# Kernel tuning notes

Hardware: AMD Instinct MI355X
Metric: run time of the kernel (lower is better)

The kernel has to match this reference:

```python
import jax, jax.numpy as jnp
import numpy as np

N = 50000   # nodes
E = 640000  # edges
IN, H, OUT = 128, 128, 64
BN_EPS = 1e-5


def setup_inputs() -> dict:
    key = jax.random.key(0)
    ks = jax.random.split(key, 16)
    inp = {}
    inp["x"] = jax.random.normal(ks[0], (N, IN), jnp.float32)
    inp["edge_index"] = jax.random.randint(ks[1], (2, E), 0, N, dtype=jnp.int32)
    # BatchNorm affine params (nontrivial so grads are informative)
    inp["bn_in_gamma"] = 1.0 + 0.1 * jax.random.normal(ks[2], (IN,), jnp.float32)
    inp["bn_in_beta"] = 0.1 * jax.random.normal(ks[3], (IN,), jnp.float32)
    inp["bn1_gamma"] = 1.0 + 0.1 * jax.random.normal(ks[4], (H,), jnp.float32)
    inp["bn1_beta"] = 0.1 * jax.random.normal(ks[5], (H,), jnp.float32)
    inp["bn2_gamma"] = 1.0 + 0.1 * jax.random.normal(ks[6], (OUT,), jnp.float32)
    inp["bn2_beta"] = 0.1 * jax.random.normal(ks[7], (OUT,), jnp.float32)
    # Linear / GCNConv weights (fan-in scaled)
    inp["proj_W"] = jax.random.normal(ks[8], (IN, H), jnp.float32) / np.sqrt(IN)
    inp["proj_b"] = jnp.zeros((H,), jnp.float32)
    inp["conv1_W"] = jax.random.normal(ks[9], (H, H), jnp.float32) / np.sqrt(H)
    inp["conv1_b"] = jnp.zeros((H,), jnp.float32)
    inp["conv2_W"] = jax.random.normal(ks[10], (H, OUT), jnp.float32) / np.sqrt(H)
    inp["conv2_b"] = jnp.zeros((OUT,), jnp.float32)
    return inp


def batchnorm(x, gamma, beta):
    # training-mode BN: batch statistics (biased variance), per-feature affine
    m = jnp.mean(x, axis=0)
    v = jnp.mean(jnp.square(x - m), axis=0)
    return (x - m) * jax.lax.rsqrt(v + BN_EPS) * gamma + beta


def gcn_conv(x, src, dst, W, b):
    # PyG GCNConv: y = D^{-1/2} (A + I) D^{-1/2} (x W) + b
    xw = x @ W                                    # [N, F_out]
    loops = jnp.arange(N, dtype=src.dtype)
    s = jnp.concatenate([src, loops])             # [E + N]
    d = jnp.concatenate([dst, loops])
    deg = jax.ops.segment_sum(jnp.ones_like(d, jnp.float32), d, num_segments=N)
    dinv = jnp.where(deg > 0, jax.lax.rsqrt(deg), 0.0)
    norm = dinv[s] * dinv[d]                      # [E + N]
    msgs = xw[s] * norm[:, None]                  # gather + per-edge scale
    out = jax.ops.segment_sum(msgs, d, num_segments=N)  # scatter-add
    return out + b


def reference(x, edge_index, bn_in_gamma, bn_in_beta, bn1_gamma, bn1_beta,
              bn2_gamma, bn2_beta, proj_W, proj_b, conv1_W, conv1_b,
              conv2_W, conv2_b):
    src, dst = edge_index[0], edge_index[1]
    h = batchnorm(x, bn_in_gamma, bn_in_beta)
    h = jax.nn.relu(h @ proj_W + proj_b)
    h = jax.nn.relu(batchnorm(gcn_conv(h, src, dst, conv1_W, conv1_b),
                              bn1_gamma, bn1_beta))
    # dropout: identity in eval mode
    out = batchnorm(gcn_conv(h, src, dst, conv2_W, conv2_b),
                    bn2_gamma, bn2_beta)
    return out
```

## Files before the change

### kernel.cpp

```cpp
#include <hip/hip_runtime.h>

#define NN 50000
#define NE 640000
#define BNEPS 1e-5f
#define NBANK 16
#define CAP 64

#define OFF_CURSOR 51200
#define OFF_ESRC 102400
#define OFF_WT0 1702400
#define OFF_WT1 1710592
#define OFF_WT2 1718784
#define OFF_STATS 1726976
#define OFF_B0 1737216
#define OFF_B1 8137216

typedef __attribute__((ext_vector_type(8))) __bf16 bf16x8;
typedef __attribute__((ext_vector_type(4))) float f32x4;

__device__ __forceinline__ float uplo(unsigned int u) {
  unsigned int v = u << 16;
  return __builtin_bit_cast(float, v);
}
__device__ __forceinline__ float uphi(unsigned int u) {
  unsigned int v = u & 0xffff0000u;
  return __builtin_bit_cast(float, v);
}
__device__ __forceinline__ unsigned int f2bf(float f) {
  unsigned int u = __builtin_bit_cast(unsigned int, f);
  return (u + 0x7fffu + ((u >> 16) & 1u)) >> 16;
}

__global__ __launch_bounds__(256) void prep_k(
    const float* __restrict__ W0, const float* __restrict__ W1,
    const float* __restrict__ W2, unsigned short* __restrict__ T0,
    unsigned short* __restrict__ T1, unsigned short* __restrict__ T2,
    int* __restrict__ cursor, float* __restrict__ stats) {
  const int bid = blockIdx.x;
  const int tid = threadIdx.x;
  if (bid < 160) {
    int f = bid * 256 + tid;
    if (f < 16384) {
      int k = f >> 7, n = f & 127;
      T0[n * 128 + k] = (unsigned short)f2bf(W0[f]);
    } else if (f < 32768) {
      int g = f - 16384;
      int k = g >> 7, n = g & 127;
      T1[n * 128 + k] = (unsigned short)f2bf(W1[g]);
    } else if (f < 40960) {
      int g = f - 32768;
      int k = g >> 6, n = g & 63;
      T2[n * 128 + k] = (unsigned short)f2bf(W2[g]);
    }
  } else if (bid < 356) {
    int i = (bid - 160) * 256 + tid;
    if (i < NN) cursor[i] = i * CAP;
  } else {
    int j = (bid - 356) * 256 + tid;
    stats[j] = 0.0f;
  }
}

template <int NC>
__device__ __forceinline__ void bn_stats_body(
    int sbid, int nsb, int tid, const float* __restrict__ A,
    float* __restrict__ sums, float* __restrict__ sqs, float (*rs)[NC],
    float (*rq)[NC]) {
  constexpr int CG = NC / 4;
  constexpr int RG = 256 / CG;
  const int tc = tid % CG;
  const int tr = tid / CG;
  float s0 = 0, s1 = 0, s2 = 0, s3 = 0, q0 = 0, q1 = 0, q2 = 0, q3 = 0;
  const int stride = nsb * RG;
  for (int r = sbid * RG + tr; r < NN; r += stride) {
    float4 v = *(const float4*)&A[(size_t)r * NC + tc * 4];
    s0 += v.x; s1 += v.y; s2 += v.z; s3 += v.w;
    q0 += v.x * v.x; q1 += v.y * v.y; q2 += v.z * v.z; q3 += v.w * v.w;
  }
  rs[tr][tc * 4] = s0; rs[tr][tc * 4 + 1] = s1;
  rs[tr][tc * 4 + 2] = s2; rs[tr][tc * 4 + 3] = s3;
  rq[tr][tc * 4] = q0; rq[tr][tc * 4 + 1] = q1;
  rq[tr][tc * 4 + 2] = q2; rq[tr][tc * 4 + 3] = q3;
  __syncthreads();
  if (tr == 0) {
    const int bank = (sbid & (NBANK - 1)) * NC;
    for (int j = 0; j < 4; ++j) {
      int c = tc * 4 + j;
      float ts = 0, tq = 0;
      for (int g = 0; g < RG; ++g) { ts += rs[g][c]; tq += rq[g][c]; }
      atomicAdd(&sums[bank + c], ts);
      atomicAdd(&sqs[bank + c], tq);
    }
  }
}

template <int NC>
__global__ __launch_bounds__(256) void bn_stats_k(const float* __restrict__ A,
                                                  float* __restrict__ sums,
                                                  float* __restrict__ sqs) {
  __shared__ float rs[256 / (NC / 4)][NC];
  __shared__ float rq[256 / (NC / 4)][NC];
  bn_stats_body<NC>(blockIdx.x, gridDim.x, threadIdx.x, A, sums, sqs, rs, rq);
}

__global__ __launch_bounds__(256) void bn_stats_bf_k(
    const unsigned short* __restrict__ Z, float* __restrict__ sums,
    float* __restrict__ sqs) {
  const int tc = threadIdx.x % 16;
  const int tr = threadIdx.x / 16;
  const int c = tc * 8;
  float s[8], q[8];
#pragma unroll
  for (int j = 0; j < 8; ++j) { s[j] = 0.f; q[j] = 0.f; }
  const int stride = gridDim.x * 16;
  for (int r = blockIdx.x * 16 + tr; r < NN; r += stride) {
    const uint4 p = *(const uint4*)&Z[(size_t)r * 128 + c];
    float e[8] = {uplo(p.x), uphi(p.x), uplo(p.y), uphi(p.y),
                  uplo(p.z), uphi(p.z), uplo(p.w), uphi(p.w)};
#pragma unroll
    for (int j = 0; j < 8; ++j) { s[j] += e[j]; q[j] += e[j] * e[j]; }
  }
  __shared__ float rs[16][128];
  __shared__ float rq[16][128];
#pragma unroll
  for (int j = 0; j < 8; ++j) { rs[tr][c + j] = s[j]; rq[tr][c + j] = q[j]; }
  __syncthreads();
  if (tr == 0) {
    const int bank = (blockIdx.x & (NBANK - 1)) * 128;
#pragma unroll
    for (int j = 0; j < 8; ++j) {
      float ts = 0.f, tq = 0.f;
      for (int g = 0; g < 16; ++g) { ts += rs[g][c + j]; tq += rq[g][c + j]; }
      atomicAdd(&sums[bank + c + j], ts);
      atomicAdd(&sqs[bank + c + j], tq);
    }
  }
}

__global__ __launch_bounds__(256) void stats_fill_k(
    const float* __restrict__ x, float* __restrict__ s0,
    float* __restrict__ q0, const int* __restrict__ src,
    const int* __restrict__ dst, int* __restrict__ cursor,
    unsigned short* __restrict__ esrc) {
  __shared__ float rs[8][128];
  __shared__ float rq[8][128];
  const int bid = blockIdx.x;
  if (bid < 1024) {
    bn_stats_body<128>(bid, 1024, threadIdx.x, x, s0, q0, rs, rq);
  } else {
    int e = (bid - 1024) * 256 + threadIdx.x;
    if (e < NE / 2) {
      int p = atomicAdd(&cursor[dst[e]], 1);
      esrc[p] = (unsigned short)src[e];
    }
  }
}

__global__ __launch_bounds__(256) void fused12_fill_k(
    const float* __restrict__ x, const unsigned short* __restrict__ Wt0,
    const unsigned short* __restrict__ Wt1, const float* __restrict__ proj_b,
    const float* __restrict__ s0, const float* __restrict__ q0,
    const float* __restrict__ g0, const float* __restrict__ b0,
    unsigned short* __restrict__ Ybf, const int* __restrict__ src,
    const int* __restrict__ dst, int* __restrict__ cursor,
    unsigned short* __restrict__ esrc) {
  __shared__ __align__(16) char smem[17408];
  __shared__ float af_s[128];
  __shared__ float bf_s[128];
  __shared__ float pb_s[128];
  const int bid = blockIdx.x;
  const int tid = threadIdx.x;
  if (bid >= 782) {
    int e = NE / 2 + (bid - 782) * 256 + tid;
    if (e < NE) {
      int p = atomicAdd(&cursor[dst[e]], 1);
      esrc[p] = (unsigned short)src[e];
    }
    return;
  }
  const int row0 = bid * 64;
  if (tid < 128) {
    float s = 0.f, q = 0.f;
#pragma unroll
    for (int b = 0; b < NBANK; ++b) {
      s += s0[b * 128 + tid];
      q += q0[b * 128 + tid];
    }
    float m = s * (1.0f / NN);
    float v = q * (1.0f / NN) - m * m;
    float a = g0[tid] * rsqrtf(v + BNEPS);
    af_s[tid] = a;
    bf_s[tid] = b0[tid] - m * a;
    pb_s[tid] = proj_b[tid];
  }
  __syncthreads();
  for (int f = tid; f < 64 * 32; f += 256) {
    const int r = f >> 5;
    const int c4 = f & 31;
    const int rg = row0 + r;
    float4 v = make_float4(0.f, 0.f, 0.f, 0.f);
    if (rg < NN) {
      v = *(const float4*)&x[(size_t)rg * 128 + c4 * 4];
      const float4 a4 = *(const float4*)&af_s[c4 * 4];
      const float4 b4 = *(const float4*)&bf_s[c4 * 4];
      v.x = fmaf(a4.x, v.x, b4.x);
      v.y = fmaf(a4.y, v.y, b4.y);
      v.z = fmaf(a4.z, v.z, b4.z);
      v.w = fmaf(a4.w, v.w, b4.w);
    }
    uint2 wv;
    wv.x = f2bf(v.x) | (f2bf(v.y) << 16);
    wv.y = f2bf(v.z) | (f2bf(v.w) << 16);
    const int ba = (r * 256 + c4 * 8) ^ ((r & 7) << 4);
    *(uint2*)(smem + ba) = wv;
  }
  __syncthreads();

  const int w = tid >> 6;
  const int l = tid & 63;
  const int lr = l & 15;
  const int lg = l >> 4;
  const int arow = w * 16 + lr;
  f32x4 acc[8];
#pragma unroll
  for (int i = 0; i < 8; ++i) acc[i] = (f32x4){0.f, 0.f, 0.f, 0.f};
#pragma unroll
  for (int kt = 0; kt < 4; ++kt) {
    const int ba = (arow * 256 + kt * 64 + lg * 16) ^ ((arow & 7) << 4);
    bf16x8 a = __builtin_bit_cast(bf16x8, *(const uint4*)(smem + ba));
#pragma unroll
    for (int nt = 0; nt < 8; ++nt) {
      bf16x8 b = __builtin_bit_cast(
          bf16x8,
          *(const uint4*)&Wt0[(size_t)(nt * 16 + lr) * 128 + kt * 32 + lg * 8]);
      acc[nt] = __builtin_amdgcn_mfma_f32_16x16x32_bf16(a, b, acc[nt], 0, 0, 0);
    }
  }
  __syncthreads();
#pragma unroll
  for (int nt = 0; nt < 8; ++nt) {
    const float pb = pb_s[nt * 16 + lr];
#pragma unroll
    for (int r = 0; r < 4; ++r) {
      const int row = w * 16 + lg * 4 + r;
      const float hv = fmaxf(acc[nt][r] + pb, 0.f);
      const int ba = (row * 256 + (nt * 16 + lr) * 2) ^ ((row & 7) << 4);
      *(unsigned short*)(smem + ba) = (unsigned short)f2bf(hv);
    }
  }
  __syncthreads();
  f32x4 acc2[8];
#pragma unroll
  for (int i = 0; i < 8; ++i) acc2[i] = (f32x4){0.f, 0.f, 0.f, 0.f};
#pragma unroll
  for (int kt = 0; kt < 4; ++kt) {
    const int ba = (arow * 256 + kt * 64 + lg * 16) ^ ((arow & 7) << 4);
    bf16x8 a = __builtin_bit_cast(bf16x8, *(const uint4*)(smem + ba));
#pragma unroll
    for (int nt = 0; nt < 8; ++nt) {
      bf16x8 b = __builtin_bit_cast(
          bf16x8,
          *(const uint4*)&Wt1[(size_t)(nt * 16 + lr) * 128 + kt * 32 + lg * 8]);
      acc2[nt] =
          __builtin_amdgcn_mfma_f32_16x16x32_bf16(a, b, acc2[nt], 0, 0, 0);
    }
  }
  float* Cl = (float*)smem;
  const int tcx = tid % 32;
  const int trx = tid / 32;
#pragma unroll
  for (int half = 0; half < 2; ++half) {
    __syncthreads();
    if ((w >> 1) == half) {
#pragma unroll
      for (int nt = 0; nt < 8; ++nt)
#pragma unroll
        for (int r = 0; r < 4; ++r)
          Cl[((w & 1) * 16 + lg * 4 + r) * 132 + nt * 16 + lr] = acc2[nt][r];
    }
    __syncthreads();
#pragma unroll
    for (int i = 0; i < 4; ++i) {
      const int rl = trx * 4 + i;
      const int rg = row0 + half * 32 + rl;
      if (rg < NN) {
        float4 v = *(const float4*)&Cl[rl * 132 + tcx * 4];
        uint2 o;
        o.x = f2bf(v.x) | (f2bf(v.y) << 16);
        o.y = f2bf(v.z) | (f2bf(v.w) << 16);
        *(uint2*)&Ybf[(size_t)rg * 128 + tcx * 4] = o;
      }
    }
  }
}

template <int NC, int OUTBF>
__global__ __launch_bounds__(256) void gather_bf_k(
    const int* __restrict__ cursor, const unsigned short* __restrict__ esrc,
    const unsigned short* __restrict__ Y, void* __restrict__ outp,
    const float* __restrict__ cb) {
  constexpr int CG = NC / 8;
  constexpr int RG = 256 / CG;
  const int tc = threadIdx.x % CG;
  const int tr = threadIdx.x / CG;
  const int n = blockIdx.x * RG + tr;
  if (n >= NN) return;
  const int c = tc * 8;
  const int beg = n * CAP;
  const int end = cursor[n];
  const float dn = rsqrtf((float)(end - beg) + 1.0f);
  float a[8];
  {
    const uint4 p = *(const uint4*)&Y[(size_t)n * NC + c];
    a[0] = dn * uplo(p.x); a[1] = dn * uphi(p.x);
    a[2] = dn * uplo(p.y); a[3] = dn * uphi(p.y);
    a[4] = dn * uplo(p.z); a[5] = dn * uphi(p.z);
    a[6] = dn * uplo(p.w); a[7] = dn * uphi(p.w);
  }
  int e = beg;
  for (; e + 2 <= end; e += 2) {
    const int s0 = esrc[e];
    const int s1 = esrc[e + 1];
    const float d0 = rsqrtf((float)(cursor[s0] - s0 * CAP) + 1.0f);
    const float d1 = rsqrtf((float)(cursor[s1] - s1 * CAP) + 1.0f);
    const uint4 q0 = *(const uint4*)&Y[(size_t)s0 * NC + c];
    const uint4 q1 = *(const uint4*)&Y[(size_t)s1 * NC + c];
    a[0] = fmaf(d0, uplo(q0.x), a[0]); a[1] = fmaf(d0, uphi(q0.x), a[1]);
    a[2] = fmaf(d0, uplo(q0.y), a[2]); a[3] = fmaf(d0, uphi(q0.y), a[3]);
    a[4] = fmaf(d0, uplo(q0.z), a[4]); a[5] = fmaf(d0, uphi(q0.z), a[5]);
    a[6] = fmaf(d0, uplo(q0.w), a[6]); a[7] = fmaf(d0, uphi(q0.w), a[7]);
    a[0] = fmaf(d1, uplo(q1.x), a[0]); a[1] = fmaf(d1, uphi(q1.x), a[1]);
    a[2] = fmaf(d1, uplo(q1.y), a[2]); a[3] = fmaf(d1, uphi(q1.y), a[3]);
    a[4] = fmaf(d1, uplo(q1.z), a[4]); a[5] = fmaf(d1, uphi(q1.z), a[5]);
    a[6] = fmaf(d1, uplo(q1.w), a[6]); a[7] = fmaf(d1, uphi(q1.w), a[7]);
  }
  if (e < end) {
    const int s0 = esrc[e];
    const float d0 = rsqrtf((float)(cursor[s0] - s0 * CAP) + 1.0f);
    const uint4 q0 = *(const uint4*)&Y[(size_t)s0 * NC + c];
    a[0] = fmaf(d0, uplo(q0.x), a[0]); a[1] = fmaf(d0, uphi(q0.x), a[1]);
    a[2] = fmaf(d0, uplo(q0.y), a[2]); a[3] = fmaf(d0, uphi(q0.y), a[3]);
    a[4] = fmaf(d0, uplo(q0.z), a[4]); a[5] = fmaf(d0, uphi(q0.z), a[5]);
    a[6] = fmaf(d0, uplo(q0.w), a[6]); a[7] = fmaf(d0, uphi(q0.w), a[7]);
  }
  float z[8];
#pragma unroll
  for (int j = 0; j < 8; ++j) z[j] = fmaf(dn, a[j], cb[c + j]);
  if constexpr (OUTBF == 1) {
    unsigned int p[4];
#pragma unroll
    for (int j = 0; j < 4; ++j)
      p[j] = f2bf(z[2 * j]) | (f2bf(z[2 * j + 1]) << 16);
    *(uint4*)&((unsigned short*)outp)[(size_t)n * NC + c] =
        make_uint4(p[0], p[1], p[2], p[3]);
  } else {
    float* Z = (float*)outp;
    *(float4*)&Z[(size_t)n * NC + c] = make_float4(z[0], z[1], z[2], z[3]);
    *(float4*)&Z[(size_t)n * NC + c + 4] = make_float4(z[4], z[5], z[6], z[7]);
  }
}

__global__ __launch_bounds__(256) void conv2_k(
    const unsigned short* __restrict__ Z1, const unsigned short* __restrict__ Wt,
    const float* __restrict__ sums, const float* __restrict__ sqs,
    const float* __restrict__ gamma, const float* __restrict__ beta,
    unsigned short* __restrict__ O1) {
  __shared__ __align__(16) char smem[16384];
  __shared__ float af_s[128];
  __shared__ float bf_s[128];
  const int tid = threadIdx.x;
  const int row0 = blockIdx.x * 64;
  if (tid < 128) {
    float s = 0.f, q = 0.f;
#pragma unroll
    for (int b = 0; b < NBANK; ++b) {
      s += sums[b * 128 + tid];
      q += sqs[b * 128 + tid];
    }
    float m = s * (1.0f / NN);
    float v = q * (1.0f / NN) - m * m;
    float a = gamma[tid] * rsqrtf(v + BNEPS);
    af_s[tid] = a;
    bf_s[tid] = beta[tid] - m * a;
  }
  __syncthreads();
  for (int f = tid; f < 64 * 16; f += 256) {
    const int r = f >> 4;
    const int c8 = f & 15;
    const int rg = row0 + r;
    uint4 w4 = make_uint4(0u, 0u, 0u, 0u);
    if (rg < NN) {
      const uint4 raw = *(const uint4*)&Z1[(size_t)rg * 128 + c8 * 8];
      const int cc = c8 * 8;
      float e[8] = {uplo(raw.x), uphi(raw.x), uplo(raw.y), uphi(raw.y),
                    uplo(raw.z), uphi(raw.z), uplo(raw.w), uphi(raw.w)};
      unsigned int p[4];
#pragma unroll
      for (int j = 0; j < 4; ++j) {
        float lo = fmaxf(fmaf(af_s[cc + 2 * j], e[2 * j], bf_s[cc + 2 * j]), 0.f);
        float hi = fmaxf(
            fmaf(af_s[cc + 2 * j + 1], e[2 * j + 1], bf_s[cc + 2 * j + 1]), 0.f);
        p[j] = f2bf(lo) | (f2bf(hi) << 16);
      }
      w4 = make_uint4(p[0], p[1], p[2], p[3]);
    }
    const int ba = (r * 256 + c8 * 16) ^ ((r & 7) << 4);
    *(uint4*)(smem + ba) = w4;
  }
  __syncthreads();
  const int w = tid >> 6;
  const int l = tid & 63;
  const int lr = l & 15;
  const int lg = l >> 4;
  const int arow = w * 16 + lr;
  f32x4 acc[4];
#pragma unroll
  for (int i = 0; i < 4; ++i) acc[i] = (f32x4){0.f, 0.f, 0.f, 0.f};
#pragma unroll
  for (int kt = 0; kt < 4; ++kt) {
    const int ba = (arow * 256 + kt * 64 + lg * 16) ^ ((arow & 7) << 4);
    bf16x8 a = __builtin_bit_cast(bf16x8, *(const uint4*)(smem + ba));
#pragma unroll
    for (int nt = 0; nt < 4; ++nt) {
      bf16x8 b = __builtin_bit_cast(
          bf16x8,
          *(const uint4*)&Wt[(size_t)(nt * 16 + lr) * 128 + kt * 32 + lg * 8]);
      acc[nt] = __builtin_amdgcn_mfma_f32_16x16x32_bf16(a, b, acc[nt], 0, 0, 0);
    }
  }
  float* Cl = (float*)smem;
  const int tcx = tid % 16;
  const int trx = tid / 16;
#pragma unroll
  for (int half = 0; half < 2; ++half) {
    __syncthreads();
    if ((w >> 1) == half) {
#pragma unroll
      for (int nt = 0; nt < 4; ++nt)
#pragma unroll
        for (int r = 0; r < 4; ++r)
          Cl[((w & 1) * 16 + lg * 4 + r) * 68 + nt * 16 + lr] = acc[nt][r];
    }
    __syncthreads();
#pragma unroll
    for (int i = 0; i < 2; ++i) {
      const int rl = trx * 2 + i;
      const int rg = row0 + half * 32 + rl;
      if (rg < NN) {
        float4 v = *(const float4*)&Cl[rl * 68 + tcx * 4];
        uint2 o;
        o.x = f2bf(v.x) | (f2bf(v.y) << 16);
        o.y = f2bf(v.z) | (f2bf(v.w) << 16);
        *(uint2*)&O1[(size_t)rg * 64 + tcx * 4] = o;
      }
    }
  }
}

__global__ __launch_bounds__(256) void final_k(
    const float* __restrict__ Z2, const float* __restrict__ s2,
    const float* __restrict__ q2, const float* __restrict__ gamma,
    const float* __restrict__ beta, float* __restrict__ out) {
  __shared__ float af_s[64];
  __shared__ float bf_s[64];
  if (threadIdx.x < 64) {
    float s = 0.f, q = 0.f;
#pragma unroll
    for (int b = 0; b < NBANK; ++b) {
      s += s2[b * 64 + threadIdx.x];
      q += q2[b * 64 + threadIdx.x];
    }
    float m = s * (1.0f / NN);
    float v = q * (1.0f / NN) - m * m;
    float a = gamma[threadIdx.x] * rsqrtf(v + BNEPS);
    af_s[threadIdx.x] = a;
    bf_s[threadIdx.x] = beta[threadIdx.x] - m * a;
  }
  __syncthreads();
  const int u = blockIdx.x * 256 + threadIdx.x;
  if (u >= NN * 16) return;
  const int r = u >> 4;
  const int c = (u & 15) * 4;
  float4 v = *(const float4*)&Z2[(size_t)r * 64 + c];
  const float4 a4 = *(const float4*)&af_s[c];
  const float4 b4 = *(const float4*)&bf_s[c];
  float4 o;
  o.x = fmaf(a4.x, v.x, b4.x);
  o.y = fmaf(a4.y, v.y, b4.y);
  o.z = fmaf(a4.z, v.z, b4.z);
  o.w = fmaf(a4.w, v.w, b4.w);
  *(float4*)&out[(size_t)r * 64 + c] = o;
}

extern "C" void kernel_launch(void* const* d_in, const int* in_sizes, int n_in,
                              void* d_out, int out_size, void* d_ws,
                              size_t ws_size, hipStream_t stream) {
  const float* x = (const float*)d_in[0];
  const int* ei = (const int*)d_in[1];
  const int* src = ei;
  const int* dst = ei + NE;
  const float* bn_in_g = (const float*)d_in[2];
  const float* bn_in_b = (const float*)d_in[3];
  const float* bn1_g = (const float*)d_in[4];
  const float* bn1_b = (const float*)d_in[5];
  const float* bn2_g = (const float*)d_in[6];
  const float* bn2_b = (const float*)d_in[7];
  const float* proj_W = (const float*)d_in[8];
  const float* proj_b = (const float*)d_in[9];
  const float* conv1_W = (const float*)d_in[10];
  const float* conv1_b = (const float*)d_in[11];
  const float* conv2_W = (const float*)d_in[12];
  const float* conv2_b = (const float*)d_in[13];
  float* out = (float*)d_out;

  float* ws = (float*)d_ws;
  int* cursor = (int*)(ws + OFF_CURSOR);
  unsigned short* esrc = (unsigned short*)(ws + OFF_ESRC);
  unsigned short* Wt0 = (unsigned short*)(ws + OFF_WT0);
  unsigned short* Wt1 = (unsigned short*)(ws + OFF_WT1);
  unsigned short* Wt2 = (unsigned short*)(ws + OFF_WT2);
  float* st = ws + OFF_STATS;
  float* s0 = st;
  float* q0 = st + 2048;
  float* s1 = st + 4096;
  float* q1 = st + 6144;
  float* s2 = st + 8192;
  float* q2 = st + 9216;
  float* B0 = ws + OFF_B0;
  float* B1 = ws + OFF_B1;
  unsigned short* Ybf = (unsigned short*)B1;
  unsigned short* Z1bf = (unsigned short*)B0;
  unsigned short* Y2bf = (unsigned short*)B1;
  float* Z2 = B0;

  prep_k<<<396, 256, 0, stream>>>(proj_W, conv1_W, conv2_W, Wt0, Wt1, Wt2,
                                  cursor, st);
  stats_fill_k<<<2274, 256, 0, stream>>>(x, s0, q0, src, dst, cursor, esrc);
  fused12_fill_k<<<2032, 256, 0, stream>>>(x, Wt0, Wt1, proj_b, s0, q0,
                                           bn_in_g, bn_in_b, Ybf, src, dst,
                                           cursor, esrc);
  gather_bf_k<128, 1><<<(NN + 15) / 16, 256, 0, stream>>>(cursor, esrc, Ybf,
                                                          Z1bf, conv1_b);
  bn_stats_bf_k<<<1024, 256, 0, stream>>>(Z1bf, s1, q1);
  conv2_k<<<782, 256, 0, stream>>>(Z1bf, Wt2, s1, q1, bn1_g, bn1_b, Y2bf);
  gather_bf_k<64, 0><<<(NN + 31) / 32, 256, 0, stream>>>(cursor, esrc, Y2bf,
                                                         Z2, conv2_b);
  bn_stats_k<64><<<1024, 256, 0, stream>>>(Z2, s2, q2);
  final_k<<<(NN * 16 + 255) / 256, 256, 0, stream>>>(Z2, s2, q2, bn2_g, bn2_b,
                                                     out);
}
```

Baseline: 169.1 us.

## Fuse BatchNorm statistics reduction into GCN gather kernels

Each gather kernel now reduces per-column sum and sum-of-squares of its output with wave shuffles and shared memory, then atomically adds into 64 banked accumulators. This removes the two separate bn_stats passes that re-read Z1 and Z2 from memory, and two kernel launches. In exchange it adds more atomics and bank reads in the consumer kernels, and workspace offsets and prep_k's zeroing grid are enlarged for the bigger stats area. A subtle point: the stats are computed from the fp32 z before bf16 rounding for Z1, which differs slightly from stats over the stored bf16 values.

```diff
diff --git a/kernel.cpp b/kernel.cpp
--- a/kernel.cpp
+++ b/kernel.cpp
@@ -4,6 +4,7 @@
 #define NE 640000
 #define BNEPS 1e-5f
 #define NBANK 16
+#define NBANKG 64
 #define CAP 64
 
 #define OFF_CURSOR 51200
@@ -12,8 +13,8 @@
 #define OFF_WT1 1710592
 #define OFF_WT2 1718784
 #define OFF_STATS 1726976
-#define OFF_B0 1737216
-#define OFF_B1 8137216
+#define OFF_B0 1755648
+#define OFF_B1 8155648
 
 typedef __attribute__((ext_vector_type(8))) __bf16 bf16x8;
 typedef __attribute__((ext_vector_type(4))) float f32x4;
@@ -94,49 +95,6 @@
   }
 }
 
-template <int NC>
-__global__ __launch_bounds__(256) void bn_stats_k(const float* __restrict__ A,
-                                                  float* __restrict__ sums,
-                                                  float* __restrict__ sqs) {
-  __shared__ float rs[256 / (NC / 4)][NC];
-  __shared__ float rq[256 / (NC / 4)][NC];
-  bn_stats_body<NC>(blockIdx.x, gridDim.x, threadIdx.x, A, sums, sqs, rs, rq);
-}
-
-__global__ __launch_bounds__(256) void bn_stats_bf_k(
-    const unsigned short* __restrict__ Z, float* __restrict__ sums,
-    float* __restrict__ sqs) {
-  const int tc = threadIdx.x % 16;
-  const int tr = threadIdx.x / 16;
-  const int c = tc * 8;
-  float s[8], q[8];
-#pragma unroll
-  for (int j = 0; j < 8; ++j) { s[j] = 0.f; q[j] = 0.f; }
-  const int stride = gridDim.x * 16;
-  for (int r = blockIdx.x * 16 + tr; r < NN; r += stride) {
-    const uint4 p = *(const uint4*)&Z[(size_t)r * 128 + c];
-    float e[8] = {uplo(p.x), uphi(p.x), uplo(p.y), uphi(p.y),
-                  uplo(p.z), uphi(p.z), uplo(p.w), uphi(p.w)};
-#pragma unroll
-    for (int j = 0; j < 8; ++j) { s[j] += e[j]; q[j] += e[j] * e[j]; }
-  }
-  __shared__ float rs[16][128];
-  __shared__ float rq[16][128];
-#pragma unroll
-  for (int j = 0; j < 8; ++j) { rs[tr][c + j] = s[j]; rq[tr][c + j] = q[j]; }
-  __syncthreads();
-  if (tr == 0) {
-    const int bank = (blockIdx.x & (NBANK - 1)) * 128;
-#pragma unroll
-    for (int j = 0; j < 8; ++j) {
-      float ts = 0.f, tq = 0.f;
-      for (int g = 0; g < 16; ++g) { ts += rs[g][c + j]; tq += rq[g][c + j]; }
-      atomicAdd(&sums[bank + c + j], ts);
-      atomicAdd(&sqs[bank + c + j], tq);
-    }
-  }
-}
-
 __global__ __launch_bounds__(256) void stats_fill_k(
     const float* __restrict__ x, float* __restrict__ s0,
     float* __restrict__ q0, const int* __restrict__ src,
@@ -298,65 +256,102 @@
 __global__ __launch_bounds__(256) void gather_bf_k(
     const int* __restrict__ cursor, const unsigned short* __restrict__ esrc,
     const unsigned short* __restrict__ Y, void* __restrict__ outp,
-    const float* __restrict__ cb) {
+    const float* __restrict__ cb, float* __restrict__ sums,
+    float* __restrict__ sqs) {
   constexpr int CG = NC / 8;
   constexpr int RG = 256 / CG;
-  const int tc = threadIdx.x % CG;
-  const int tr = threadIdx.x / CG;
+  __shared__ float ws_s[4][NC];
+  __shared__ float ws_q[4][NC];
+  const int tid = threadIdx.x;
+  const int tc = tid % CG;
+  const int tr = tid / CG;
   const int n = blockIdx.x * RG + tr;
-  if (n >= NN) return;
+  const bool act = (n < NN);
   const int c = tc * 8;
-  const int beg = n * CAP;
-  const int end = cursor[n];
-  const float dn = rsqrtf((float)(end - beg) + 1.0f);
-  float a[8];
-  {
-    const uint4 p = *(const uint4*)&Y[(size_t)n * NC + c];
-    a[0] = dn * uplo(p.x); a[1] = dn * uphi(p.x);
-    a[2] = dn * uplo(p.y); a[3] = dn * uphi(p.y);
-    a[4] = dn * uplo(p.z); a[5] = dn * uphi(p.z);
-    a[6] = dn * uplo(p.w); a[7] = dn * uphi(p.w);
-  }
-  int e = beg;
-  for (; e + 2 <= end; e += 2) {
-    const int s0 = esrc[e];
-    const int s1 = esrc[e + 1];
-    const float d0 = rsqrtf((float)(cursor[s0] - s0 * CAP) + 1.0f);
-    const float d1 = rsqrtf((float)(cursor[s1] - s1 * CAP) + 1.0f);
-    const uint4 q0 = *(const uint4*)&Y[(size_t)s0 * NC + c];
-    const uint4 q1 = *(const uint4*)&Y[(size_t)s1 * NC + c];
-    a[0] = fmaf(d0, uplo(q0.x), a[0]); a[1] = fmaf(d0, uphi(q0.x), a[1]);
-    a[2] = fmaf(d0, uplo(q0.y), a[2]); a[3] = fmaf(d0, uphi(q0.y), a[3]);
-    a[4] = fmaf(d0, uplo(q0.z), a[4]); a[5] = fmaf(d0, uphi(q0.z), a[5]);
-    a[6] = fmaf(d0, uplo(q0.w), a[6]); a[7] = fmaf(d0, uphi(q0.w), a[7]);
-    a[0] = fmaf(d1, uplo(q1.x), a[0]); a[1] = fmaf(d1, uphi(q1.x), a[1]);
-    a[2] = fmaf(d1, uplo(q1.y), a[2]); a[3] = fmaf(d1, uphi(q1.y), a[3]);
-    a[4] = fmaf(d1, uplo(q1.z), a[4]); a[5] = fmaf(d1, uphi(q1.z), a[5]);
-    a[6] = fmaf(d1, uplo(q1.w), a[6]); a[7] = fmaf(d1, uphi(q1.w), a[7]);
-  }
-  if (e < end) {
-    const int s0 = esrc[e];
-    const float d0 = rsqrtf((float)(cursor[s0] - s0 * CAP) + 1.0f);
-    const uint4 q0 = *(const uint4*)&Y[(size_t)s0 * NC + c];
-    a[0] = fmaf(d0, uplo(q0.x), a[0]); a[1] = fmaf(d0, uphi(q0.x), a[1]);
-    a[2] = fmaf(d0, uplo(q0.y), a[2]); a[3] = fmaf(d0, uphi(q0.y), a[3]);
-    a[4] = fmaf(d0, uplo(q0.z), a[4]); a[5] = fmaf(d0, uphi(q0.z), a[5]);
-    a[6] = fmaf(d0, uplo(q0.w), a[6]); a[7] = fmaf(d0, uphi(q0.w), a[7]);
-  }
   float z[8];
 #pragma unroll
-  for (int j = 0; j < 8; ++j) z[j] = fmaf(dn, a[j], cb[c + j]);
-  if constexpr (OUTBF == 1) {
-    unsigned int p[4];
-#pragma unroll
-    for (int j = 0; j < 4; ++j)
-      p[j] = f2bf(z[2 * j]) | (f2bf(z[2 * j + 1]) << 16);
-    *(uint4*)&((unsigned short*)outp)[(size_t)n * NC + c] =
-        make_uint4(p[0], p[1], p[2], p[3]);
-  } else {
-    float* Z = (float*)outp;
-    *(float4*)&Z[(size_t)n * NC + c] = make_float4(z[0], z[1], z[2], z[3]);
-    *(float4*)&Z[(size_t)n * NC + c + 4] = make_float4(z[4], z[5], z[6], z[7]);
+  for (int j = 0; j < 8; ++j) z[j] = 0.f;
+  if (act) {
+    const int beg = n * CAP;
+    const int end = cursor[n];
+    const float dn = rsqrtf((float)(end - beg) + 1.0f);
+    float a[8];
+    {
+      const uint4 p = *(const uint4*)&Y[(size_t)n * NC + c];
+      a[0] = dn * uplo(p.x); a[1] = dn * uphi(p.x);
+      a[2] = dn * uplo(p.y); a[3] = dn * uphi(p.y);
+      a[4] = dn * uplo(p.z); a[5] = dn * uphi(p.z);
+      a[6] = dn * uplo(p.w); a[7] = dn * uphi(p.w);
+    }
+    int e = beg;
+    for (; e + 2 <= end; e += 2) {
+      const int s0 = esrc[e];
+      const int s1 = esrc[e + 1];
+      const float d0 = rsqrtf((float)(cursor[s0] - s0 * CAP) + 1.0f);
+      const float d1 = rsqrtf((float)(cursor[s1] - s1 * CAP) + 1.0f);
+      const uint4 q0 = *(const uint4*)&Y[(size_t)s0 * NC + c];
+      const uint4 q1 = *(const uint4*)&Y[(size_t)s1 * NC + c];
+      a[0] = fmaf(d0, uplo(q0.x), a[0]); a[1] = fmaf(d0, uphi(q0.x), a[1]);
+      a[2] = fmaf(d0, uplo(q0.y), a[2]); a[3] = fmaf(d0, uphi(q0.y), a[3]);
+      a[4] = fmaf(d0, uplo(q0.z), a[4]); a[5] = fmaf(d0, uphi(q0.z), a[5]);
+      a[6] = fmaf(d0, uplo(q0.w), a[6]); a[7] = fmaf(d0, uphi(q0.w), a[7]);
+      a[0] = fmaf(d1, uplo(q1.x), a[0]); a[1] = fmaf(d1, uphi(q1.x), a[1]);
+      a[2] = fmaf(d1, uplo(q1.y), a[2]); a[3] = fmaf(d1, uphi(q1.y), a[3]);
+      a[4] = fmaf(d1, uplo(q1.z), a[4]); a[5] = fmaf(d1, uphi(q1.z), a[5]);
+      a[6] = fmaf(d1, uplo(q1.w), a[6]); a[7] = fmaf(d1, uphi(q1.w), a[7]);
+    }
+    if (e < end) {
+      const int s0 = esrc[e];
+      const float d0 = rsqrtf((float)(cursor[s0] - s0 * CAP) + 1.0f);
+      const uint4 q0 = *(const uint4*)&Y[(size_t)s0 * NC + c];
+      a[0] = fmaf(d0, uplo(q0.x), a[0]); a[1] = fmaf(d0, uphi(q0.x), a[1]);
+      a[2] = fmaf(d0, uplo(q0.y), a[2]); a[3] = fmaf(d0, uphi(q0.y), a[3]);
+      a[4] = fmaf(d0, uplo(q0.z), a[4]); a[5] = fmaf(d0, uphi(q0.z), a[5]);
+      a[6] = fmaf(d0, uplo(q0.w), a[6]); a[7] = fmaf(d0, uphi(q0.w), a[7]);
+    }
+#pragma unroll
+    for (int j = 0; j < 8; ++j) z[j] = fmaf(dn, a[j], cb[c + j]);
+    if constexpr (OUTBF == 1) {
+      unsigned int p[4];
+#pragma unroll
+      for (int j = 0; j < 4; ++j)
+        p[j] = f2bf(z[2 * j]) | (f2bf(z[2 * j + 1]) << 16);
+      *(uint4*)&((unsigned short*)outp)[(size_t)n * NC + c] =
+          make_uint4(p[0], p[1], p[2], p[3]);
+    } else {
+      float* Z = (float*)outp;
+      *(float4*)&Z[(size_t)n * NC + c] = make_float4(z[0], z[1], z[2], z[3]);
+      *(float4*)&Z[(size_t)n * NC + c + 4] =
+          make_float4(z[4], z[5], z[6], z[7]);
+    }
+  }
+  float s[8], q[8];
+#pragma unroll
+  for (int j = 0; j < 8; ++j) { s[j] = z[j]; q[j] = z[j] * z[j]; }
+#pragma unroll
+  for (int off = CG; off < 64; off <<= 1) {
+#pragma unroll
+    for (int j = 0; j < 8; ++j) {
+      s[j] += __shfl_xor(s[j], off);
+      q[j] += __shfl_xor(q[j], off);
+    }
+  }
+  const int w = tid >> 6;
+  const int l = tid & 63;
+  if (l < CG) {
+    *(float4*)&ws_s[w][c] = make_float4(s[0], s[1], s[2], s[3]);
+    *(float4*)&ws_s[w][c + 4] = make_float4(s[4], s[5], s[6], s[7]);
+    *(float4*)&ws_q[w][c] = make_float4(q[0], q[1], q[2], q[3]);
+    *(float4*)&ws_q[w][c + 4] = make_float4(q[4], q[5], q[6], q[7]);
+  }
+  __syncthreads();
+  if (tid < NC) {
+    float ts = 0.f, tq = 0.f;
+#pragma unroll
+    for (int g = 0; g < 4; ++g) { ts += ws_s[g][tid]; tq += ws_q[g][tid]; }
+    const int bank = (blockIdx.x % NBANKG) * NC;
+    atomicAdd(&sums[bank + tid], ts);
+    atomicAdd(&sqs[bank + tid], tq);
   }
 }
 
@@ -373,7 +368,7 @@
   if (tid < 128) {
     float s = 0.f, q = 0.f;
 #pragma unroll
-    for (int b = 0; b < NBANK; ++b) {
+    for (int b = 0; b < NBANKG; ++b) {
       s += sums[b * 128 + tid];
       q += sqs[b * 128 + tid];
     }
@@ -466,7 +461,7 @@
   if (threadIdx.x < 64) {
     float s = 0.f, q = 0.f;
 #pragma unroll
-    for (int b = 0; b < NBANK; ++b) {
+    for (int b = 0; b < NBANKG; ++b) {
       s += s2[b * 64 + threadIdx.x];
       q += q2[b * 64 + threadIdx.x];
     }
@@ -523,9 +518,9 @@
   float* s0 = st;
   float* q0 = st + 2048;
   float* s1 = st + 4096;
-  float* q1 = st + 6144;
-  float* s2 = st + 8192;
-  float* q2 = st + 9216;
+  float* q1 = st + 12288;
+  float* s2 = st + 20480;
+  float* q2 = st + 24576;
   float* B0 = ws + OFF_B0;
   float* B1 = ws + OFF_B1;
   unsigned short* Ybf = (unsigned short*)B1;
@@ -533,19 +528,17 @@
   unsigned short* Y2bf = (unsigned short*)B1;
   float* Z2 = B0;
 
-  prep_k<<<396, 256, 0, stream>>>(proj_W, conv1_W, conv2_W, Wt0, Wt1, Wt2,
+  prep_k<<<468, 256, 0, stream>>>(proj_W, conv1_W, conv2_W, Wt0, Wt1, Wt2,
                                   cursor, st);
   stats_fill_k<<<2274, 256, 0, stream>>>(x, s0, q0, src, dst, cursor, esrc);
   fused12_fill_k<<<2032, 256, 0, stream>>>(x, Wt0, Wt1, proj_b, s0, q0,
                                            bn_in_g, bn_in_b, Ybf, src, dst,
                                            cursor, esrc);
-  gather_bf_k<128, 1><<<(NN + 15) / 16, 256, 0, stream>>>(cursor, esrc, Ybf,
-                                                          Z1bf, conv1_b);
-  bn_stats_bf_k<<<1024, 256, 0, stream>>>(Z1bf, s1, q1);
+  gather_bf_k<128, 1><<<3125, 256, 0, stream>>>(cursor, esrc, Ybf, Z1bf,
+                                                conv1_b, s1, q1);
   conv2_k<<<782, 256, 0, stream>>>(Z1bf, Wt2, s1, q1, bn1_g, bn1_b, Y2bf);
-  gather_bf_k<64, 0><<<(NN + 31) / 32, 256, 0, stream>>>(cursor, esrc, Y2bf,
-                                                         Z2, conv2_b);
-  bn_stats_k<64><<<1024, 256, 0, stream>>>(Z2, s2, q2);
+  gather_bf_k<64, 0><<<1563, 256, 0, stream>>>(cursor, esrc, Y2bf, Z2, conv2_b,
+                                               s2, q2);
   final_k<<<(NN * 16 + 255) / 256, 256, 0, stream>>>(Z2, s2, q2, bn2_g, bn2_b,
                                                      out);
 }
```

Measured after the change: 150.3 us. -11.1%, faster.
